# Kernel tuning notes

Hardware: AMD Instinct MI355X
Metric: run time of the kernel (lower is better)

The kernel has to match this reference:

```python
import jax, jax.numpy as jnp
import numpy as np
import math

L, E, NH, P, MLP_H, OUT = 4, 512, 8, 16, 2048, 1024
HD = E // NH
EPS = 1e-6

def layernorm(x, g, b):
    mu = jnp.mean(x, axis=-1, keepdims=True)
    var = jnp.mean(jnp.square(x - mu), axis=-1, keepdims=True)
    return g * (x - mu) / jnp.sqrt(var + EPS) + b

def gelu_tanh(x):
    c = jnp.float32(0.7978845608028654)
    return 0.5 * x * (1.0 + jnp.tanh(c * (x + 0.044715 * x * x * x)))

def sinusoidal_pos(T, dim):
    pos = jnp.arange(T, dtype=jnp.float32)[:, None]
    div = jnp.exp(jnp.arange(0, dim, 2, dtype=jnp.float32) * (-math.log(10000.0) / dim))
    pe = jnp.concatenate([jnp.sin(pos * div), jnp.cos(pos * div)], axis=1)
    return pe[:, :dim]  # [T, dim] (all sins then all cos, matching source)

def _heads(y, B, T):
    return jnp.transpose(y.reshape(B, T, NH, HD), (0, 2, 1, 3))  # [B,H,T,D]

def self_attn(x, Wqkv, Wo):
    B, T, _ = x.shape
    q, k, v = jnp.split(x @ Wqkv, 3, axis=-1)
    q, k, v = _heads(q, B, T), _heads(k, B, T), _heads(v, B, T)
    logits = jnp.einsum('bhqd,bhkd->bhqk', q, k) * (HD ** -0.5)
    attn = jax.nn.softmax(logits, axis=-1)
    out = jnp.einsum('bhqk,bhkd->bhqd', attn, v)
    out = jnp.transpose(out, (0, 2, 1, 3)).reshape(B, T, E)
    return out @ Wo

def cross_attn(xq, xkv, Wq, Wkv, Wo):
    B, Tq, _ = xq.shape
    Tk = xkv.shape[1]
    q = _heads(xq @ Wq, B, Tq)
    k, v = jnp.split(xkv @ Wkv, 2, axis=-1)
    k, v = _heads(k, B, Tk), _heads(v, B, Tk)
    logits = jnp.einsum('bhqd,bhkd->bhqk', q, k) * (HD ** -0.5)
    attn = jax.nn.softmax(logits, axis=-1)
    out = jnp.einsum('bhqk,bhkd->bhqd', attn, v)
    out = jnp.transpose(out, (0, 2, 1, 3)).reshape(B, Tq, E)
    return out @ Wo

def block(x, i, ln1_g, ln1_b, Wqkv, Wo, ln2_g, ln2_b, W1, b1, W2, b2):
    x = x + self_attn(layernorm(x, ln1_g[i], ln1_b[i]), Wqkv[i], Wo[i])
    h = layernorm(x, ln2_g[i], ln2_b[i])
    h = gelu_tanh(h @ W1[i] + b1[i]) @ W2[i] + b2[i]
    return x + h

def setup_inputs():
    key = jax.random.key(0)
    ks = jax.random.split(key, 16)
    B, HW = 8, 512
    w = lambda k, sh: jax.random.normal(k, sh, dtype=jnp.float32) * 0.02
    return {
        'img1': jax.random.normal(ks[0], (B, HW, HW, 3), dtype=jnp.float32),
        'img2': jax.random.normal(ks[1], (B, HW, HW, 3), dtype=jnp.float32),
        'patch_W': w(ks[2], (P, P, 3, E)),
        'cls_token': w(ks[3], (1, 1, E)),
        'cls_pos': w(ks[4], (1, 1, E)),
        'ln1_g': jnp.ones((L, E)), 'ln1_b': jnp.zeros((L, E)),
        'Wqkv': w(ks[5], (L, E, 3 * E)),
        'Wo': w(ks[6], (L, E, E)),
        'ln2_g': jnp.ones((L, E)), 'ln2_b': jnp.zeros((L, E)),
        'W1': w(ks[7], (L, E, MLP_H)), 'b1': jnp.zeros((L, MLP_H)),
        'W2': w(ks[8], (L, MLP_H, E)), 'b2': jnp.zeros((L, E)),
        'Wq_c': w(ks[9], (E, E)),
        'Wkv_c': w(ks[10], (E, 2 * E)),
        'Wo_c': w(ks[11], (E, E)),
        'nf_g': jnp.ones((E,)), 'nf_b': jnp.zeros((E,)),
        'Wdec': w(ks[12], (E, OUT)), 'bdec': jnp.zeros((OUT,)),
    }

def reference(img1, img2, patch_W, cls_token, cls_pos, ln1_g, ln1_b, Wqkv, Wo,
              ln2_g, ln2_b, W1, b1, W2, b2, Wq_c, Wkv_c, Wo_c, nf_g, nf_b, Wdec, bdec):
    B = img1.shape[0]
    def embed(img):
        p = jax.lax.conv_general_dilated(img, patch_W, (P, P), 'SAME',
                                         dimension_numbers=('NHWC', 'HWIO', 'NHWC'))
        Bh, Hh, Wh, C = p.shape
        t = p.reshape(Bh, Hh * Wh, C)
        return t + sinusoidal_pos(Hh * Wh, C)[None]
    t1, t2 = embed(img1), embed(img2)
    cls = jnp.tile(cls_token + cls_pos, (B, 1, 1))
    x1 = jnp.concatenate([cls, t1], axis=1)
    x2 = jnp.concatenate([cls, t2], axis=1)
    for i in range(L):
        x1 = block(x1, i, ln1_g, ln1_b, Wqkv, Wo, ln2_g, ln2_b, W1, b1, W2, b2)
        x2 = block(x2, i, ln1_g, ln1_b, Wqkv, Wo, ln2_g, ln2_b, W1, b1, W2, b2)
    cls1, tok1 = x1[:, :1, :], x1[:, 1:, :]
    cls2, tok2 = x2[:, :1, :], x2[:, 1:, :]
    cls1 = cls1 + cross_attn(cls1, tok2, Wq_c, Wkv_c, Wo_c)
    cls2 = cls2 + cross_attn(cls2, tok1, Wq_c, Wkv_c, Wo_c)
    cls_avg = 0.5 * (cls1[:, 0, :] + cls2[:, 0, :])
    cls_avg = layernorm(cls_avg, nf_g, nf_b)
    y = cls_avg @ Wdec + bdec
    return y[:, None, None, :]  # [B,1,1,1024]
```

## Files before the change

### kernel.cpp

```cpp
#include <hip/hip_runtime.h>
#include <stdint.h>
#include <math.h>

typedef __attribute__((ext_vector_type(4))) float f4;
typedef __attribute__((ext_vector_type(8))) __bf16 bf8;
typedef __attribute__((ext_vector_type(8))) short s8;
typedef __attribute__((ext_vector_type(4))) uint32_t u32x4;

#define DI __device__ __forceinline__

DI short f2bf(float f){
  union { float f; uint32_t u; } v; v.f = f;
  uint32_t r = v.u + 0x7fffu + ((v.u >> 16) & 1u);
  return (short)(r >> 16);
}
DI float bf2f(short s){
  union { uint32_t u; float f; } v; v.u = ((uint32_t)(uint16_t)s) << 16;
  return v.f;
}
DI uint32_t cvtpk(float lo, float hi){
  uint32_t r;
  asm("v_cvt_pk_bf16_f32 %0, %1, %2" : "=v"(r) : "v"(lo), "v"(hi));
  return r;
}
DI float gelu_f(float u){
  float z = 1.5957691216057308f * u * fmaf(0.044715f, u*u, 1.f);
  return u * __builtin_amdgcn_rcpf(1.f + __expf(-z));
}
DI void gload16(const void* g, void* l){
  __builtin_amdgcn_global_load_lds((const __attribute__((address_space(1))) unsigned*)g,
                                   (__attribute__((address_space(3))) unsigned*)l, 16, 0, 0);
}

__global__ __launch_bounds__(256)
void k_transpose(const float* __restrict__ in, short* __restrict__ out, int K, int N, size_t stride)
{
  __shared__ float t[32][33];
  in  += (size_t)blockIdx.z * stride;
  out += (size_t)blockIdx.z * stride;
  int n0 = blockIdx.x*32, k0 = blockIdx.y*32;
  int tx = threadIdx.x, ty = threadIdx.y;
  #pragma unroll
  for (int i=0;i<32;i+=8) t[ty+i][tx] = in[(size_t)(k0+ty+i)*N + n0+tx];
  __syncthreads();
  #pragma unroll
  for (int i=0;i<32;i+=8) out[(size_t)(n0+ty+i)*K + k0+tx] = f2bf(t[tx][ty+i]);
}

__global__ void k_pe(float* __restrict__ pe)
{
  int p = blockIdx.x;
  for (int d = threadIdx.x; d < 512; d += 256){
    int j = (d < 256) ? d : d - 256;
    float div = expf((float)(2*j) * (-9.210340371976184f/512.f));
    float a = (float)p * div;
    pe[(size_t)p*512 + d] = (d < 256) ? sinf(a) : cosf(a);
  }
}

__global__ __launch_bounds__(256)
void k_gather(const float* __restrict__ img1, const float* __restrict__ img2, short* __restrict__ patches)
{
  int row = blockIdx.x;
  int img = row >> 13;
  int b   = (row >> 10) & 7;
  int p   = row & 1023;
  int ph = p >> 5, pw = p & 31;
  const float* src = (img ? img2 : img1) + (size_t)b*512*512*3;
  short* dst = patches + (size_t)row*768;
  for (int k = threadIdx.x; k < 768; k += 256){
    int i = k / 48; int rem = k - i*48; int j = rem / 3; int c = rem - j*3;
    int yy = ph*16 + i, xx = pw*16 + j;
    dst[k] = f2bf(src[((size_t)yy*512 + xx)*3 + c]);
  }
}

__global__ void k_zeropad(float* __restrict__ x)
{
  int idx = blockIdx.x; int ib = idx / 31; int t = 1025 + (idx - ib*31);
  x[((size_t)ib*1056 + t)*512 + threadIdx.x] = 0.f;
}
__global__ void k_cls(const float* __restrict__ ct, const float* __restrict__ cp, float* __restrict__ x)
{
  int ib = blockIdx.x; int e = threadIdx.x;
  x[(size_t)ib*1056*512 + e] = ct[e] + cp[e];
}

__global__ __launch_bounds__(256)
void k_layernorm(const float* __restrict__ x, short* __restrict__ y,
                 const float* __restrict__ g, const float* __restrict__ b)
{
  int row = blockIdx.x*4 + (threadIdx.x>>6);
  int l = threadIdx.x & 63;
  const float* xr = x + (size_t)row*512 + l*8;
  f4 v0 = *(const f4*)xr;
  f4 v1 = *(const f4*)(xr+4);
  float s = v0[0]+v0[1]+v0[2]+v0[3]+v1[0]+v1[1]+v1[2]+v1[3];
  float q = v0[0]*v0[0]+v0[1]*v0[1]+v0[2]*v0[2]+v0[3]*v0[3]
          + v1[0]*v1[0]+v1[1]*v1[1]+v1[2]*v1[2]+v1[3]*v1[3];
  #pragma unroll
  for (int m=1;m<64;m<<=1){ s += __shfl_xor(s,m); q += __shfl_xor(q,m); }
  float mu = s * 0.001953125f;
  float var = q * 0.001953125f - mu*mu;
  float rstd = rsqrtf(var + 1e-6f);
  const float* gp = g + l*8;
  const float* bp = b + l*8;
  float ov[8];
  #pragma unroll
  for (int j=0;j<8;j++){
    float xv = (j<4) ? v0[j] : v1[j-4];
    ov[j] = gp[j]*(xv-mu)*rstd + bp[j];
  }
  u32x4 pk;
  #pragma unroll
  for (int j=0;j<4;j++) pk[j] = cvtpk(ov[2*j], ov[2*j+1]);
  *(u32x4*)(y + (size_t)row*512 + l*8) = pk;
}

__global__ void k_cast_bf16(const float* __restrict__ in, short* __restrict__ out)
{
  size_t i = (size_t)blockIdx.x*256 + threadIdx.x;
  const float* p = in + i*8;
  u32x4 pk;
  #pragma unroll
  for (int j=0;j<4;j++) pk[j] = cvtpk(p[2*j], p[2*j+1]);
  *(u32x4*)(out + i*8) = pk;
}

struct EpiArgs { short* outb; float* outf; const float* bias; const float* pe; short* vT; };

template<int EPI>
__global__ __launch_bounds__(256)
void k_gemm(const short* __restrict__ A, const short* __restrict__ Bt,
            int M, int N, int K, EpiArgs ea)
{
  __shared__ short Al[128*64];
  __shared__ short Bl[128*64];
  const int tid = threadIdx.x;
  const int l = tid & 63;
  const int w = tid >> 6;
  const int wr = (w >> 1) * 64, wc = (w & 1) * 64;
  const int lr = l & 15, lg = l >> 4;
  const int brow = blockIdx.y * 128, bcol = blockIdx.x * 128;
  const short* Ab = A  + (size_t)brow * K;
  const short* Bb = Bt + (size_t)bcol * K;
  f4 acc[4][4];
  #pragma unroll
  for (int m=0;m<4;m++)
    #pragma unroll
    for (int n=0;n<4;n++){ acc[m][n][0]=0.f; acc[m][n][1]=0.f; acc[m][n][2]=0.f; acc[m][n][3]=0.f; }

  const int rsw = lr & 7;
  for (int kt = 0; kt < K; kt += 64){
    #pragma unroll
    for (int i=0;i<4;i++){
      int s   = i*256 + tid;
      int row = s >> 3;
      int gs  = (s & 7) ^ (row & 7);
      gload16(Ab + (size_t)row*K + kt + gs*8, &Al[s*8]);
      gload16(Bb + (size_t)row*K + kt + gs*8, &Bl[s*8]);
    }
    __syncthreads();
    #pragma unroll
    for (int ko=0;ko<2;ko++){
      bf8 af[4], bfr[4];
      const int ps = ((ko*4 + lg) ^ rsw) * 8;
      #pragma unroll
      for (int m=0;m<4;m++) af[m]  = *(const bf8*)&Al[(wr + m*16 + lr)*64 + ps];
      #pragma unroll
      for (int n=0;n<4;n++) bfr[n] = *(const bf8*)&Bl[(wc + n*16 + lr)*64 + ps];
      #pragma unroll
      for (int m=0;m<4;m++)
        #pragma unroll
        for (int n=0;n<4;n++)
          acc[m][n] = __builtin_amdgcn_mfma_f32_16x16x32_bf16(af[m], bfr[n], acc[m][n], 0, 0, 0);
    }
    __syncthreads();
  }

  #pragma unroll
  for (int m=0;m<4;m++){
    #pragma unroll
    for (int n=0;n<4;n++){
      const int row0 = brow + wr + m*16 + lg*4;
      const int col  = bcol + wc + n*16 + lr;
      float v0 = acc[m][n][0], v1 = acc[m][n][1], v2 = acc[m][n][2], v3 = acc[m][n][3];
      if (EPI == 0 || EPI == 1){
        if (EPI == 1 && col < 512){ v0*=0.125f; v1*=0.125f; v2*=0.125f; v3*=0.125f; }
        uint32_t u01 = cvtpk(v0, v1), u23 = cvtpk(v2, v3);
        short s0 = (short)u01, s1 = (short)(u01>>16), s2 = (short)u23, s3 = (short)(u23>>16);
        ea.outb[(size_t)(row0+0)*N + col] = s0;
        ea.outb[(size_t)(row0+1)*N + col] = s1;
        ea.outb[(size_t)(row0+2)*N + col] = s2;
        ea.outb[(size_t)(row0+3)*N + col] = s3;
        if (EPI == 1 && col >= 1024){
          int ib = row0 / 1056, t = row0 - ib*1056;
          short* vtb = ea.vT + ((size_t)ib*512 + (col - 1024))*1056;
          vtb[t] = s0; vtb[t+1] = s1; vtb[t+2] = s2; vtb[t+3] = s3;
        }
      } else if (EPI == 2){
        float bv = ea.bias ? ea.bias[col] : 0.f;
        ea.outf[(size_t)(row0+0)*N + col] += v0 + bv;
        ea.outf[(size_t)(row0+1)*N + col] += v1 + bv;
        ea.outf[(size_t)(row0+2)*N + col] += v2 + bv;
        ea.outf[(size_t)(row0+3)*N + col] += v3 + bv;
      } else if (EPI == 3){
        float bv = ea.bias[col];
        float g0 = gelu_f(v0+bv), g1 = gelu_f(v1+bv), g2 = gelu_f(v2+bv), g3 = gelu_f(v3+bv);
        uint32_t u01 = cvtpk(g0, g1), u23 = cvtpk(g2, g3);
        ea.outb[(size_t)(row0+0)*N + col] = (short)u01;
        ea.outb[(size_t)(row0+1)*N + col] = (short)(u01>>16);
        ea.outb[(size_t)(row0+2)*N + col] = (short)u23;
        ea.outb[(size_t)(row0+3)*N + col] = (short)(u23>>16);
      } else if (EPI == 4){
        #pragma unroll
        for (int r=0;r<4;r++){
          int row = row0 + r;
          int ib = row >> 10, p = row & 1023;
          float v = (r==0)?v0:(r==1)?v1:(r==2)?v2:v3;
          ea.outf[((size_t)(ib*1056 + 1 + p))*512 + col] = v + ea.pe[(size_t)p*512 + col];
        }
      }
    }
  }
}

__global__ __launch_bounds__(256)
void k_attn(const short* __restrict__ qkv, const short* __restrict__ vT, short* __restrict__ aout)
{
  __shared__ __align__(16) short Kl[2][32*64];
  __shared__ __align__(16) short Vl[2][64*32];
  __shared__ short Pl[4][2][32*40];
  __shared__ float Sc[4][2][32];

  const int tid = threadIdx.x;
  const int w  = tid >> 6;
  const int qtR = blockIdx.x * 4 + w;
  const int qt  = qtR > 32 ? 32 : qtR;
  const int u  = blockIdx.y;
  const int ib = u >> 3, h = u & 7;
  const int l = tid & 63, lr = l & 15, lg = l >> 4;
  const size_t rb = (size_t)ib * 1056;
  const int t0 = qt * 32;

  bf8 qf[2][2];
  #pragma unroll
  for (int nq=0;nq<2;nq++)
    #pragma unroll
    for (int ks=0;ks<2;ks++)
      qf[nq][ks] = *(const bf8*)&qkv[(rb + t0 + nq*16 + lr)*1536 + h*64 + ks*32 + lg*8];

  f4 o[2][4];
  float mrun[2], lrun[2];
  #pragma unroll
  for (int mq=0;mq<2;mq++)
    #pragma unroll
    for (int nd=0;nd<4;nd++){ o[mq][nd][0]=0.f; o[mq][nd][1]=0.f; o[mq][nd][2]=0.f; o[mq][nd][3]=0.f; }
  mrun[0]=mrun[1]=-1e30f; lrun[0]=lrun[1]=0.f;

  auto STAGE = [&](int buf, int jt){
    const int j0 = jt*32;
    {
      int krow = tid >> 3, ks = tid & 7;
      int gs = ks ^ (krow & 7);
      gload16(&qkv[(rb + j0 + krow)*1536 + 512 + h*64 + gs*8], &Kl[buf][tid*8]);
    }
    {
      int vrow = tid >> 2, vs = tid & 3;
      int gs = vs ^ (vrow & 3);
      gload16(&vT[((size_t)ib*512 + h*64 + vrow)*1056 + j0 + gs*8], &Vl[buf][tid*8]);
    }
  };

  STAGE(0, 0);

  for (int jt=0; jt<=32; jt++){
    const int cur = jt & 1;
    const int pb  = cur;
    const bool MASK = (jt == 32);
    const int j0 = jt*32;
    __syncthreads();

    bf8 kc[2][2], vb[4];
    #pragma unroll
    for (int mk=0;mk<2;mk++)
      #pragma unroll
      for (int ks=0;ks<2;ks++)
        kc[mk][ks] = *(const bf8*)&Kl[cur][((mk*16+lr)*8 + ((ks*4+lg) ^ (lr&7)))*8];
    #pragma unroll
    for (int nd=0;nd<4;nd++)
      vb[nd] = *(const bf8*)&Vl[cur][((nd*16+lr)*4 + (lg ^ (lr&3)))*8];

    if (jt < 32) STAGE(cur^1, jt+1);

    f4 st[2][2];
    #pragma unroll
    for (int mk=0;mk<2;mk++)
      #pragma unroll
      for (int nq=0;nq<2;nq++){ st[mk][nq][0]=0.f; st[mk][nq][1]=0.f; st[mk][nq][2]=0.f; st[mk][nq][3]=0.f; }
    __builtin_amdgcn_s_setprio(1);
    #pragma unroll
    for (int ks=0;ks<2;ks++)
      #pragma unroll
      for (int mk=0;mk<2;mk++)
        #pragma unroll
        for (int nq=0;nq<2;nq++)
          st[mk][nq] = __builtin_amdgcn_mfma_f32_16x16x32_bf16(kc[mk][ks], qf[nq][ks], st[mk][nq], 0, 0, 0);
    __builtin_amdgcn_s_setprio(0);

    float p8[2][8], mx[2];
    #pragma unroll
    for (int nq=0;nq<2;nq++){
      mx[nq] = -1e30f;
      #pragma unroll
      for (int mk=0;mk<2;mk++)
        #pragma unroll
        for (int r=0;r<4;r++){
          float v = st[mk][nq][r];
          if (MASK){
            int kk = j0 + mk*16 + lg*4 + r;
            v = (kk > 1024) ? -1e30f : v;
          }
          p8[nq][mk*4+r] = v;
          mx[nq] = fmaxf(mx[nq], v);
        }
      mx[nq] = fmaxf(mx[nq], __shfl_xor(mx[nq], 16));
      mx[nq] = fmaxf(mx[nq], __shfl_xor(mx[nq], 32));
    }

    bool ok = (mx[0] <= mrun[0] + 8.f) && (mx[1] <= mrun[1] + 8.f);
    if (__all(ok)){
      #pragma unroll
      for (int nq=0;nq<2;nq++){
        float rs = 0.f;
        #pragma unroll
        for (int i=0;i<8;i++){ float p = __expf(p8[nq][i] - mrun[nq]); p8[nq][i] = p; rs += p; }
        rs += __shfl_xor(rs, 16);
        rs += __shfl_xor(rs, 32);
        lrun[nq] += rs;
        uint32_t* prow = (uint32_t*)&Pl[w][pb][(nq*16 + lr)*40];
        #pragma unroll
        for (int mk=0;mk<2;mk++){
          prow[mk*8 + lg*2]     = cvtpk(p8[nq][mk*4+0], p8[nq][mk*4+1]);
          prow[mk*8 + lg*2 + 1] = cvtpk(p8[nq][mk*4+2], p8[nq][mk*4+3]);
        }
      }
      asm volatile("s_waitcnt lgkmcnt(0)" ::: "memory");
      __builtin_amdgcn_sched_barrier(0);
      bf8 pa[2];
      #pragma unroll
      for (int mq=0;mq<2;mq++) pa[mq] = *(const bf8*)&Pl[w][pb][(mq*16 + lr)*40 + lg*8];
      __builtin_amdgcn_s_setprio(1);
      #pragma unroll
      for (int mq=0;mq<2;mq++)
        #pragma unroll
        for (int nd=0;nd<4;nd++)
          o[mq][nd] = __builtin_amdgcn_mfma_f32_16x16x32_bf16(pa[mq], vb[nd], o[mq][nd], 0, 0, 0);
      __builtin_amdgcn_s_setprio(0);
    } else {
      #pragma unroll
      for (int nq=0;nq<2;nq++){
        float mn = fmaxf(mrun[nq], mx[nq]);
        float sc = __expf(mrun[nq] - mn);
        mrun[nq] = mn;
        float rs = 0.f;
        #pragma unroll
        for (int i=0;i<8;i++){ float p = __expf(p8[nq][i] - mn); p8[nq][i] = p; rs += p; }
        rs += __shfl_xor(rs, 16);
        rs += __shfl_xor(rs, 32);
        lrun[nq] = lrun[nq]*sc + rs;
        Sc[w][pb][nq*16 + lr] = sc;
        uint32_t* prow = (uint32_t*)&Pl[w][pb][(nq*16 + lr)*40];
        #pragma unroll
        for (int mk=0;mk<2;mk++){
          prow[mk*8 + lg*2]     = cvtpk(p8[nq][mk*4+0], p8[nq][mk*4+1]);
          prow[mk*8 + lg*2 + 1] = cvtpk(p8[nq][mk*4+2], p8[nq][mk*4+3]);
        }
      }
      asm volatile("s_waitcnt lgkmcnt(0)" ::: "memory");
      __builtin_amdgcn_sched_barrier(0);
      f4 scv[2]; bf8 pa[2];
      #pragma unroll
      for (int mq=0;mq<2;mq++){
        scv[mq] = *(const f4*)&Sc[w][pb][mq*16 + lg*4];
        pa[mq]  = *(const bf8*)&Pl[w][pb][(mq*16 + lr)*40 + lg*8];
      }
      #pragma unroll
      for (int mq=0;mq<2;mq++)
        #pragma unroll
        for (int nd=0;nd<4;nd++){
          #pragma unroll
          for (int r=0;r<4;r++) o[mq][nd][r] *= scv[mq][r];
        }
      __builtin_amdgcn_s_setprio(1);
      #pragma unroll
      for (int mq=0;mq<2;mq++)
        #pragma unroll
        for (int nd=0;nd<4;nd++)
          o[mq][nd] = __builtin_amdgcn_mfma_f32_16x16x32_bf16(pa[mq], vb[nd], o[mq][nd], 0, 0, 0);
      __builtin_amdgcn_s_setprio(0);
    }
  }

  if (qtR <= 32){
    #pragma unroll
    for (int nq=0;nq<2;nq++) Sc[w][1][nq*16 + lr] = lrun[nq];
    asm volatile("s_waitcnt lgkmcnt(0)" ::: "memory");
    __builtin_amdgcn_sched_barrier(0);
    #pragma unroll
    for (int mq=0;mq<2;mq++){
      f4 lsv = *(const f4*)&Sc[w][1][mq*16 + lg*4];
      float i0 = __builtin_amdgcn_rcpf(lsv[0]);
      float i1 = __builtin_amdgcn_rcpf(lsv[1]);
      float i2 = __builtin_amdgcn_rcpf(lsv[2]);
      float i3 = __builtin_amdgcn_rcpf(lsv[3]);
      const size_t base = rb + t0 + mq*16 + lg*4;
      #pragma unroll
      for (int nd=0;nd<4;nd++){
        int col = h*64 + nd*16 + lr;
        uint32_t u01 = cvtpk(o[mq][nd][0]*i0, o[mq][nd][1]*i1);
        uint32_t u23 = cvtpk(o[mq][nd][2]*i2, o[mq][nd][3]*i3);
        aout[(base+0)*512 + col] = (short)u01;
        aout[(base+1)*512 + col] = (short)(u01>>16);
        aout[(base+2)*512 + col] = (short)u23;
        aout[(base+3)*512 + col] = (short)(u23>>16);
      }
    }
  }
}

__global__ __launch_bounds__(256)
void k_cross_q(const float* __restrict__ x, const float* __restrict__ Wq, float* __restrict__ qc)
{
  __shared__ float xs[512];
  int ib = blockIdx.x;
  const float* xr = x + (size_t)ib*1056*512;
  for (int e=threadIdx.x;e<512;e+=256) xs[e] = xr[e];
  __syncthreads();
  for (int n=threadIdx.x;n<512;n+=256){
    float acc = 0.f;
    for (int k=0;k<512;k++) acc += xs[k]*Wq[(size_t)k*512 + n];
    qc[(size_t)ib*512 + n] = acc;
  }
}

__global__ __launch_bounds__(64)
void k_cross_attn(const float* __restrict__ qc, const short* __restrict__ kv, float* __restrict__ oc)
{
  int u = blockIdx.x; int ib = u >> 3, h = u & 7;
  int img = ib >> 3, b = ib & 7;
  int sib = (1 - img)*8 + b;
  int l = threadIdx.x;
  __shared__ float qs[64];
  __shared__ float pl[1024];
  qs[l] = qc[(size_t)ib*512 + h*64 + l];
  __syncthreads();
  float lmax = -1e30f;
  for (int jj=0; jj<16; jj++){
    int j = jj*64 + l;
    const short* kr = kv + ((size_t)(sib*1056 + 1 + j))*1024 + h*64;
    float acc = 0.f;
    for (int d=0; d<64; d++) acc += qs[d]*bf2f(kr[d]);
    acc *= 0.125f;
    pl[j] = acc;
    lmax = fmaxf(lmax, acc);
  }
  #pragma unroll
  for (int m=1;m<64;m<<=1) lmax = fmaxf(lmax, __shfl_xor(lmax, m));
  __syncthreads();
  float lsum = 0.f;
  for (int jj=0; jj<16; jj++){
    int j = jj*64 + l;
    float p = __expf(pl[j] - lmax);
    pl[j] = p; lsum += p;
  }
  #pragma unroll
  for (int m=1;m<64;m<<=1) lsum += __shfl_xor(lsum, m);
  __syncthreads();
  float acc = 0.f;
  for (int j=0;j<1024;j++)
    acc += pl[j] * bf2f(kv[((size_t)(sib*1056 + 1 + j))*1024 + 512 + h*64 + l]);
  oc[(size_t)ib*512 + h*64 + l] = acc / lsum;
}

__global__ __launch_bounds__(256)
void k_cross_out(const float* __restrict__ x, const float* __restrict__ oc,
                 const float* __restrict__ Wo, float* __restrict__ cn)
{
  __shared__ float os[512];
  int ib = blockIdx.x;
  for (int e=threadIdx.x;e<512;e+=256) os[e] = oc[(size_t)ib*512+e];
  __syncthreads();
  for (int n=threadIdx.x;n<512;n+=256){
    float acc = 0.f;
    for (int k=0;k<512;k++) acc += os[k]*Wo[(size_t)k*512+n];
    cn[(size_t)ib*512+n] = x[(size_t)ib*1056*512 + n] + acc;
  }
}

__global__ __launch_bounds__(256)
void k_final(const float* __restrict__ cn, const float* __restrict__ nfg, const float* __restrict__ nfb,
             const float* __restrict__ Wdec, const float* __restrict__ bdec, float* __restrict__ out)
{
  int b = blockIdx.x;
  __shared__ float a[512];
  __shared__ float an[512];
  __shared__ float red[8];
  int tid = threadIdx.x;
  float s = 0.f, q = 0.f;
  for (int e=tid;e<512;e+=256){
    float av = 0.5f*(cn[(size_t)b*512 + e] + cn[(size_t)(8+b)*512 + e]);
    a[e] = av; s += av; q += av*av;
  }
  #pragma unroll
  for (int m=1;m<64;m<<=1){ s += __shfl_xor(s,m); q += __shfl_xor(q,m); }
  int w = tid>>6;
  if ((tid&63)==0){ red[w] = s; red[4+w] = q; }
  __syncthreads();
  s = red[0]+red[1]+red[2]+red[3];
  q = red[4]+red[5]+red[6]+red[7];
  float mu = s*0.001953125f;
  float var = q*0.001953125f - mu*mu;
  float rstd = rsqrtf(var + 1e-6f);
  for (int e=tid;e<512;e+=256) an[e] = nfg[e]*(a[e]-mu)*rstd + nfb[e];
  __syncthreads();
  for (int n=tid;n<1024;n+=256){
    float acc = bdec[n];
    for (int e=0;e<512;e++) acc += an[e]*Wdec[(size_t)e*1024 + n];
    out[(size_t)b*1024 + n] = acc;
  }
}

extern "C" void kernel_launch(void* const* d_in, const int* in_sizes, int n_in,
                              void* d_out, int out_size, void* d_ws, size_t ws_size,
                              hipStream_t stream)
{
  (void)in_sizes; (void)n_in;
  const float* img1 = (const float*)d_in[0];
  const float* img2 = (const float*)d_in[1];
  const float* patchW = (const float*)d_in[2];
  const float* cls_t = (const float*)d_in[3];
  const float* cls_p = (const float*)d_in[4];
  const float* ln1g = (const float*)d_in[5];
  const float* ln1b = (const float*)d_in[6];
  const float* Wqkv = (const float*)d_in[7];
  const float* Wo   = (const float*)d_in[8];
  const float* ln2g = (const float*)d_in[9];
  const float* ln2b = (const float*)d_in[10];
  const float* W1   = (const float*)d_in[11];
  const float* b1   = (const float*)d_in[12];
  const float* W2   = (const float*)d_in[13];
  const float* b2   = (const float*)d_in[14];
  const float* Wqc  = (const float*)d_in[15];
  const float* Wkvc = (const float*)d_in[16];
  const float* Woc  = (const float*)d_in[17];
  const float* nfg  = (const float*)d_in[18];
  const float* nfb  = (const float*)d_in[19];
  const float* Wdec = (const float*)d_in[20];
  const float* bdec = (const float*)d_in[21];
  float* out = (float*)d_out;

  const size_t offA = 34603008, offB = 51904512, offC = 121110528, offD = 148111360;
  const size_t NEEDED = 148209664;
  if (ws_size < NEEDED){
    hipMemsetAsync(d_out, 0, (size_t)out_size*sizeof(float), stream);
    return;
  }
  char* ws = (char*)d_ws;
  float* x    = (float*)ws;
  short* y    = (short*)(ws + offA);
  short* attn = y;
  short* qkv  = (short*)(ws + offB);
  short* vT   = (short*)(ws + offB + 51904512);
  short* mh   = (short*)(ws + offB);
  short* patches = (short*)(ws + offB);
  float* pe   = (float*)(ws + offB + 25165824);
  short* kvc  = (short*)(ws + offB);
  short* wts  = (short*)(ws + offC);
  float* qc   = (float*)(ws + offD);
  float* oc   = (float*)(ws + offD + 32768);
  float* cn   = (float*)(ws + offD + 65536);

  short* patchWt = wts;
  short* WqkvT = wts + 393216;
  short* WoT   = wts + 3538944;
  short* W1T   = wts + 4587520;
  short* W2T   = wts + 8781824;
  short* WkvT  = wts + 12976128;

  dim3 tb(32,8,1);
  k_transpose<<<dim3(16,24,1), tb, 0, stream>>>(patchW, patchWt, 768, 512, (size_t)768*512);
  k_transpose<<<dim3(48,16,4), tb, 0, stream>>>(Wqkv, WqkvT, 512, 1536, (size_t)512*1536);
  k_transpose<<<dim3(16,16,4), tb, 0, stream>>>(Wo,   WoT,   512, 512,  (size_t)512*512);
  k_transpose<<<dim3(64,16,4), tb, 0, stream>>>(W1,   W1T,   512, 2048, (size_t)512*2048);
  k_transpose<<<dim3(16,64,4), tb, 0, stream>>>(W2,   W2T,   2048, 512, (size_t)2048*512);
  k_transpose<<<dim3(32,16,1), tb, 0, stream>>>(Wkvc, WkvT,  512, 1024, (size_t)512*1024);

  k_pe<<<1024, 256, 0, stream>>>(pe);
  k_gather<<<16384, 256, 0, stream>>>(img1, img2, patches);
  k_zeropad<<<496, 512, 0, stream>>>(x);
  k_cls<<<16, 512, 0, stream>>>(cls_t, cls_p, x);

  EpiArgs ea;
  ea = EpiArgs{nullptr, x, nullptr, pe, nullptr};
  k_gemm<4><<<dim3(4, 128), 256, 0, stream>>>(patches, patchWt, 16384, 512, 768, ea);

  for (int i=0;i<4;i++){
    k_layernorm<<<4224, 256, 0, stream>>>(x, y, ln1g + i*512, ln1b + i*512);
    ea = EpiArgs{qkv, nullptr, nullptr, nullptr, vT};
    k_gemm<1><<<dim3(12, 132), 256, 0, stream>>>(y, WqkvT + (size_t)i*1536*512, 16896, 1536, 512, ea);
    k_attn<<<dim3(9, 128), 256, 0, stream>>>(qkv, vT, attn);
    ea = EpiArgs{nullptr, x, nullptr, nullptr, nullptr};
    k_gemm<2><<<dim3(4, 132), 256, 0, stream>>>(attn, WoT + (size_t)i*512*512, 16896, 512, 512, ea);
    k_layernorm<<<4224, 256, 0, stream>>>(x, y, ln2g + i*512, ln2b + i*512);
    ea = EpiArgs{mh, nullptr, b1 + i*2048, nullptr, nullptr};
    k_gemm<3><<<dim3(16, 132), 256, 0, stream>>>(y, W1T + (size_t)i*2048*512, 16896, 2048, 512, ea);
    ea = EpiArgs{nullptr, x, b2 + i*512, nullptr, nullptr};
    k_gemm<2><<<dim3(4, 132), 256, 0, stream>>>(mh, W2T + (size_t)i*512*2048, 16896, 512, 2048, ea);
  }

  k_cast_bf16<<<4224, 256, 0, stream>>>(x, y);
  ea = EpiArgs{kvc, nullptr, nullptr, nullptr, nullptr};
  k_gemm<0><<<dim3(8, 132), 256, 0, stream>>>(y, WkvT, 16896, 1024, 512, ea);
  k_cross_q<<<16, 256, 0, stream>>>(x, Wqc, qc);
  k_cross_attn<<<128, 64, 0, stream>>>(qc, kvc, oc);
  k_cross_out<<<16, 256, 0, stream>>>(x, oc, Woc, cn);
  k_final<<<8, 256, 0, stream>>>(cn, nfg, nfb, Wdec, bdec, out);
}
```

Baseline: 1.623 ms.

## Swizzle GEMM tiles across XCDs, fold log2e into Q scale, parallelize final

GEMM launches become 1D grids whose block index is remapped so consecutive tiles land on the same XCD, improving L2 locality of shared A/B panels. The Q scaling now includes log2(e) so attention softmax uses exp2f, with the deferred-rescale threshold scaled to match. The final decoder projection is split over 64 blocks instead of 8, with each block recomputing the layernorm. The swizzle assumes grid sizes are divisible by 8.

```diff
diff --git a/kernel.cpp b/kernel.cpp
--- a/kernel.cpp
+++ b/kernel.cpp
@@ -132,7 +132,7 @@
 template<int EPI>
 __global__ __launch_bounds__(256)
 void k_gemm(const short* __restrict__ A, const short* __restrict__ Bt,
-            int M, int N, int K, EpiArgs ea)
+            int M, int N, int K, int gridX, EpiArgs ea)
 {
   __shared__ short Al[128*64];
   __shared__ short Bl[128*64];
@@ -141,7 +141,10 @@
   const int w = tid >> 6;
   const int wr = (w >> 1) * 64, wc = (w & 1) * 64;
   const int lr = l & 15, lg = l >> 4;
-  const int brow = blockIdx.y * 128, bcol = blockIdx.x * 128;
+  const int nwg = gridDim.x;
+  const int q8 = nwg >> 3;
+  const int nb = (blockIdx.x & 7) * q8 + (blockIdx.x >> 3);
+  const int brow = (nb / gridX) * 128, bcol = (nb % gridX) * 128;
   const short* Ab = A  + (size_t)brow * K;
   const short* Bb = Bt + (size_t)bcol * K;
   f4 acc[4][4];
@@ -186,7 +189,10 @@
       const int col  = bcol + wc + n*16 + lr;
       float v0 = acc[m][n][0], v1 = acc[m][n][1], v2 = acc[m][n][2], v3 = acc[m][n][3];
       if (EPI == 0 || EPI == 1){
-        if (EPI == 1 && col < 512){ v0*=0.125f; v1*=0.125f; v2*=0.125f; v3*=0.125f; }
+        if (EPI == 1 && col < 512){
+          const float qs = 0.1803368801111204f;
+          v0*=qs; v1*=qs; v2*=qs; v3*=qs;
+        }
         uint32_t u01 = cvtpk(v0, v1), u23 = cvtpk(v2, v3);
         short s0 = (short)u01, s1 = (short)(u01>>16), s2 = (short)u23, s3 = (short)(u23>>16);
         ea.outb[(size_t)(row0+0)*N + col] = s0;
@@ -242,6 +248,7 @@
   const int l = tid & 63, lr = l & 15, lg = l >> 4;
   const size_t rb = (size_t)ib * 1056;
   const int t0 = qt * 32;
+  const float DEFER_THR = 11.541560327111707f;
 
   bf8 qf[2][2];
   #pragma unroll
@@ -328,13 +335,13 @@
       mx[nq] = fmaxf(mx[nq], __shfl_xor(mx[nq], 32));
     }
 
-    bool ok = (mx[0] <= mrun[0] + 8.f) && (mx[1] <= mrun[1] + 8.f);
+    bool ok = (mx[0] <= mrun[0] + DEFER_THR) && (mx[1] <= mrun[1] + DEFER_THR);
     if (__all(ok)){
       #pragma unroll
       for (int nq=0;nq<2;nq++){
         float rs = 0.f;
         #pragma unroll
-        for (int i=0;i<8;i++){ float p = __expf(p8[nq][i] - mrun[nq]); p8[nq][i] = p; rs += p; }
+        for (int i=0;i<8;i++){ float p = exp2f(p8[nq][i] - mrun[nq]); p8[nq][i] = p; rs += p; }
         rs += __shfl_xor(rs, 16);
         rs += __shfl_xor(rs, 32);
         lrun[nq] += rs;
@@ -361,11 +368,11 @@
       #pragma unroll
       for (int nq=0;nq<2;nq++){
         float mn = fmaxf(mrun[nq], mx[nq]);
-        float sc = __expf(mrun[nq] - mn);
+        float sc = exp2f(mrun[nq] - mn);
         mrun[nq] = mn;
         float rs = 0.f;
         #pragma unroll
-        for (int i=0;i<8;i++){ float p = __expf(p8[nq][i] - mn); p8[nq][i] = p; rs += p; }
+        for (int i=0;i<8;i++){ float p = exp2f(p8[nq][i] - mn); p8[nq][i] = p; rs += p; }
         rs += __shfl_xor(rs, 16);
         rs += __shfl_xor(rs, 32);
         lrun[nq] = lrun[nq]*sc + rs;
@@ -502,15 +509,15 @@
 void k_final(const float* __restrict__ cn, const float* __restrict__ nfg, const float* __restrict__ nfb,
              const float* __restrict__ Wdec, const float* __restrict__ bdec, float* __restrict__ out)
 {
-  int b = blockIdx.x;
-  __shared__ float a[512];
+  int b = blockIdx.x >> 3;
+  int n0 = (blockIdx.x & 7) * 128;
   __shared__ float an[512];
   __shared__ float red[8];
   int tid = threadIdx.x;
   float s = 0.f, q = 0.f;
   for (int e=tid;e<512;e+=256){
     float av = 0.5f*(cn[(size_t)b*512 + e] + cn[(size_t)(8+b)*512 + e]);
-    a[e] = av; s += av; q += av*av;
+    an[e] = av; s += av; q += av*av;
   }
   #pragma unroll
   for (int m=1;m<64;m<<=1){ s += __shfl_xor(s,m); q += __shfl_xor(q,m); }
@@ -522,12 +529,13 @@
   float mu = s*0.001953125f;
   float var = q*0.001953125f - mu*mu;
   float rstd = rsqrtf(var + 1e-6f);
-  for (int e=tid;e<512;e+=256) an[e] = nfg[e]*(a[e]-mu)*rstd + nfb[e];
-  __syncthreads();
-  for (int n=tid;n<1024;n+=256){
-    float acc = bdec[n];
-    for (int e=0;e<512;e++) acc += an[e]*Wdec[(size_t)e*1024 + n];
-    out[(size_t)b*1024 + n] = acc;
+  for (int e=tid;e<512;e+=256) an[e] = nfg[e]*(an[e]-mu)*rstd + nfb[e];
+  __syncthreads();
+  for (int n=tid;n<128;n+=256){
+    int col = n0 + n;
+    float acc = bdec[col];
+    for (int e=0;e<512;e++) acc += an[e]*Wdec[(size_t)e*1024 + col];
+    out[(size_t)b*1024 + col] = acc;
   }
 }
 
@@ -603,27 +611,27 @@
 
   EpiArgs ea;
   ea = EpiArgs{nullptr, x, nullptr, pe, nullptr};
-  k_gemm<4><<<dim3(4, 128), 256, 0, stream>>>(patches, patchWt, 16384, 512, 768, ea);
+  k_gemm<4><<<512, 256, 0, stream>>>(patches, patchWt, 16384, 512, 768, 4, ea);
 
   for (int i=0;i<4;i++){
     k_layernorm<<<4224, 256, 0, stream>>>(x, y, ln1g + i*512, ln1b + i*512);
     ea = EpiArgs{qkv, nullptr, nullptr, nullptr, vT};
-    k_gemm<1><<<dim3(12, 132), 256, 0, stream>>>(y, WqkvT + (size_t)i*1536*512, 16896, 1536, 512, ea);
+    k_gemm<1><<<1584, 256, 0, stream>>>(y, WqkvT + (size_t)i*1536*512, 16896, 1536, 512, 12, ea);
     k_attn<<<dim3(9, 128), 256, 0, stream>>>(qkv, vT, attn);
     ea = EpiArgs{nullptr, x, nullptr, nullptr, nullptr};
-    k_gemm<2><<<dim3(4, 132), 256, 0, stream>>>(attn, WoT + (size_t)i*512*512, 16896, 512, 512, ea);
+    k_gemm<2><<<528, 256, 0, stream>>>(attn, WoT + (size_t)i*512*512, 16896, 512, 512, 4, ea);
     k_layernorm<<<4224, 256, 0, stream>>>(x, y, ln2g + i*512, ln2b + i*512);
     ea = EpiArgs{mh, nullptr, b1 + i*2048, nullptr, nullptr};
-    k_gemm<3><<<dim3(16, 132), 256, 0, stream>>>(y, W1T + (size_t)i*2048*512, 16896, 2048, 512, ea);
+    k_gemm<3><<<2112, 256, 0, stream>>>(y, W1T + (size_t)i*2048*512, 16896, 2048, 512, 16, ea);
     ea = EpiArgs{nullptr, x, b2 + i*512, nullptr, nullptr};
-    k_gemm<2><<<dim3(4, 132), 256, 0, stream>>>(mh, W2T + (size_t)i*512*2048, 16896, 512, 2048, ea);
+    k_gemm<2><<<528, 256, 0, stream>>>(mh, W2T + (size_t)i*512*2048, 16896, 512, 2048, 4, ea);
   }
 
   k_cast_bf16<<<4224, 256, 0, stream>>>(x, y);
   ea = EpiArgs{kvc, nullptr, nullptr, nullptr, nullptr};
-  k_gemm<0><<<dim3(8, 132), 256, 0, stream>>>(y, WkvT, 16896, 1024, 512, ea);
+  k_gemm<0><<<1056, 256, 0, stream>>>(y, WkvT, 16896, 1024, 512, 8, ea);
   k_cross_q<<<16, 256, 0, stream>>>(x, Wqc, qc);
   k_cross_attn<<<128, 64, 0, stream>>>(qc, kvc, oc);
   k_cross_out<<<16, 256, 0, stream>>>(x, oc, Woc, cn);
-  k_final<<<8, 256, 0, stream>>>(cn, nfg, nfb, Wdec, bdec, out);
-}
+  k_final<<<64, 256, 0, stream>>>(cn, nfg, nfb, Wdec, bdec, out);
+}
```

New measurement: 1.578 ms. 2.8% less time.
